# Kernel optimization log

Measured on AMD Instinct MI355X. Metric: run time of the kernel, lower is better.

The kernel has to match this reference:

```python
import jax, jax.numpy as jnp
import numpy as np

B, P, C, H, W = 256, 512, 512, 7, 8
T = H * W  # 56
EPS = 1e-8


def setup_inputs() -> dict:
    key = jax.random.key(0)
    k1, k2, k3 = jax.random.split(key, 3)
    inp = jax.random.normal(k1, (B, C, H, W), dtype=jnp.float32)
    # xavier-uniform-like init for prototype (fan over last two dims as torch does)
    bound_p = float(np.sqrt(6.0 / (P + C * T)))
    prototype = jax.random.uniform(k2, (P, C, T), dtype=jnp.float32, minval=-bound_p, maxval=bound_p)
    bound_w = float(np.sqrt(6.0 / (C + 1)))
    fc_w = jax.random.uniform(k3, (1, C), dtype=jnp.float32, minval=-bound_w, maxval=bound_w)
    fc_b = jnp.zeros((1,), dtype=jnp.float32)
    return {"input": inp, "prototype": prototype, "fc_w": fc_w, "fc_b": fc_b}


def reference(input, prototype, fc_w, fc_b):
    # flatten spatial dims: (B, C, T)
    x = input.reshape(input.shape[0], input.shape[1], -1)
    # per-position cosine similarity over channel dim
    dots = jnp.einsum('bct,pct->bpt', x, prototype)          # (B, P, T)
    xn = jnp.linalg.norm(x, axis=1)                           # (B, T)
    pn = jnp.linalg.norm(prototype, axis=1)                   # (P, T)
    sim = dots / jnp.maximum(xn[:, None, :] * pn[None, :, :], EPS)
    att = jax.nn.softmax(sim, axis=-1)                        # (B, P, T)
    # attention-pooled elementwise product: (B, P, C)
    feat = jnp.einsum('bpt,bct,pct->bpc', att, x, prototype)
    # fc: Linear(C, 1) then relu, view to (B, P)
    out = jax.nn.relu(jnp.einsum('bpc,oc->bpo', feat, fc_w) + fc_b)
    return out.reshape(out.shape[0], out.shape[1])
```

## Files before the change

### kernel.cpp

```cpp
#include <hip/hip_runtime.h>
#include <hip/hip_bf16.h>
#include <math.h>

constexpr int kB = 256, kC = 512, kT = 56, kP = 512;
constexpr int kCT = kC * kT;

typedef short v4s __attribute__((ext_vector_type(4)));
typedef short v8s __attribute__((ext_vector_type(8)));
typedef float v4f __attribute__((ext_vector_type(4)));

__device__ __forceinline__ unsigned pack_bf16(float a, float b) {
  __hip_bfloat16 ha = __float2bfloat16(a);
  __hip_bfloat16 hb = __float2bfloat16(b);
  unsigned short ua, ub;
  __builtin_memcpy(&ua, &ha, 2);
  __builtin_memcpy(&ub, &hb, 2);
  return (unsigned)ua | ((unsigned)ub << 16);
}

__device__ __forceinline__ v4s frag2(unsigned w0, unsigned w1) {
  unsigned u[2] = {w0, w1};
  v4s s;
  __builtin_memcpy(&s, u, 8);
  return s;
}

__device__ __forceinline__ v8s frag8(uint4 u) {
  v8s s;
  __builtin_memcpy(&s, &u, 16);
  return s;
}

__global__ __launch_bounds__(512) void prep_kernel(
    const float* __restrict__ x, const float* __restrict__ proto,
    const float* __restrict__ fcw,
    unsigned* __restrict__ xt, unsigned* __restrict__ xwt,
    unsigned* __restrict__ pt,
    float* __restrict__ xn, float* __restrict__ pn) {
  __shared__ float tile[512 * 57];
  __shared__ float fws[512];
  __shared__ float part[8][64];

  const int tid = threadIdx.x;
  const int n = blockIdx.x;
  const bool isx = (n < kB);
  const int row = isx ? n : (n - kB);
  const float* src = (isx ? x + (size_t)row * kCT : proto + (size_t)row * kCT);

  fws[tid] = fcw[tid & 511];

#pragma unroll 1
  for (int it = 0; it < 14; ++it) {
    const int f0 = it * 2048 + tid * 4;
    float4 v = *(const float4*)(src + f0);
#pragma unroll
    for (int j = 0; j < 4; ++j) {
      int f = f0 + j;
      int c = (int)(((unsigned)f * 74899u) >> 22);
      int t = f - c * 56;
      tile[c * 57 + t] = ((const float*)&v)[j];
    }
  }
  __syncthreads();

  {
    const int g = tid >> 6, tt = tid & 63;
    float a = 0.f;
    if (tt < 56) {
      for (int c = g * 64; c < g * 64 + 64; ++c) {
        float u = tile[c * 57 + tt];
        a = fmaf(u, u, a);
      }
    }
    part[g][tt] = a;
  }
  __syncthreads();
  if (tid < 56) {
    float s = 0.f;
#pragma unroll
    for (int g = 0; g < 8; ++g) s += part[g][tid];
    float r = sqrtf(s);
    if (isx) xn[row * 56 + tid] = r; else pn[row * 56 + tid] = r;
  }

#pragma unroll 1
  for (int it = 0; it < 28; ++it) {
    const int id = it * 512 + tid;
    const int t = id >> 8;
    const int cw = id & 255;
    float g0 = tile[(2 * cw) * 57 + t];
    float g1 = tile[(2 * cw + 1) * 57 + t];
    unsigned wd = pack_bf16(g0, g1);
    if (isx) {
      size_t o = ((size_t)(t * kB + row)) * 256 + cw;
      xt[o] = wd;
      xwt[o] = pack_bf16(g0 * fws[2 * cw], g1 * fws[2 * cw + 1]);
    } else {
      pt[((size_t)(t * kP + row)) * 256 + cw] = wd;
    }
  }
}

constexpr int TSZ = 64 * 64;
constexpr int BUF = 3 * TSZ;

__global__ __launch_bounds__(512) void proto_gemm_kernel(
    const unsigned* __restrict__ xt, const unsigned* __restrict__ xwt,
    const unsigned* __restrict__ pt,
    const float* __restrict__ xn, const float* __restrict__ pn,
    float* __restrict__ part) {
  __shared__ __align__(16) unsigned lds[2 * BUF];

  const int tid = threadIdx.x;
  const int l = tid & 63;
  const int w = tid >> 6;
  const int wm = w & 3;
  const int wn = w >> 2;
  const int b0 = blockIdx.x * 64;
  const int p0 = blockIdx.y * 64;
  const int tg = blockIdx.z;

  const int sr0 = tid >> 4;
  const int sr1 = sr0 + 32;
  const int sc = (tid & 15) * 4;
  const int lw0 = sr0 * 64 + (sc ^ ((sr0 & 7) * 4));
  const int lw1 = sr1 * 64 + (sc ^ ((sr1 & 7) * 4));

  const int fr = l & 15;
  const int q = l >> 4;
  const int sw = (fr & 7) * 4;
  const int axr = (wm * 16 + fr) * 64;
  const int ap0r = (wn * 32 + fr) * 64;
  const int ap1r = ap0r + 16 * 64;

  v4f aD0, aD1, aW0, aW1;
  aD0 = aD1 = aW0 = aW1 = v4f{0.f, 0.f, 0.f, 0.f};
  v4f m0v, m1v, s0v, s1v, n0v, n1v;
  m0v = m1v = v4f{-3.0e38f, -3.0e38f, -3.0e38f, -3.0e38f};
  s0v = s1v = n0v = n1v = v4f{0.f, 0.f, 0.f, 0.f};

  uint4 Ax0, Ax1, Aw0, Aw1, Ap0, Ap1;
  uint4 Bx0, Bx1, Bw0, Bw1, Bp0, Bp1;
  float xnv[4] = {0.f, 0.f, 0.f, 0.f};
  float pnv0 = 0.f, pnv1 = 0.f;

#define LOAD_REGS(S, CC) do { \
    const int t_ = tg * 7 + ((CC) >> 2); \
    const int w0_ = ((CC) & 3) * 64; \
    const unsigned* gx_ = xt + ((size_t)(t_ * kB + b0)) * 256 + w0_ + sc; \
    const unsigned* gw_ = xwt + ((size_t)(t_ * kB + b0)) * 256 + w0_ + sc; \
    const unsigned* gp_ = pt + ((size_t)(t_ * kP + p0)) * 256 + w0_ + sc; \
    S##x0 = *(const uint4*)(gx_ + (size_t)sr0 * 256); \
    S##x1 = *(const uint4*)(gx_ + (size_t)sr1 * 256); \
    S##w0 = *(const uint4*)(gw_ + (size_t)sr0 * 256); \
    S##w1 = *(const uint4*)(gw_ + (size_t)sr1 * 256); \
    S##p0 = *(const uint4*)(gp_ + (size_t)sr0 * 256); \
    S##p1 = *(const uint4*)(gp_ + (size_t)sr1 * 256); \
  } while (0)

#define STORE_LDS(S, CC) do { \
    unsigned* b_ = lds + ((CC) & 1) * BUF; \
    *(uint4*)(b_ + lw0) = S##x0; \
    *(uint4*)(b_ + lw1) = S##x1; \
    *(uint4*)(b_ + TSZ + lw0) = S##w0; \
    *(uint4*)(b_ + TSZ + lw1) = S##w1; \
    *(uint4*)(b_ + 2 * TSZ + lw0) = S##p0; \
    *(uint4*)(b_ + 2 * TSZ + lw1) = S##p1; \
  } while (0)

  auto compute = [&](int cc) {
    if ((cc & 3) == 0) {
      const int t = tg * 7 + (cc >> 2);
      const int brow = b0 + wm * 16 + q * 4;
#pragma unroll
      for (int i = 0; i < 4; ++i) xnv[i] = xn[(brow + i) * 56 + t];
      pnv0 = pn[(p0 + wn * 32 + fr) * 56 + t];
      pnv1 = pn[(p0 + wn * 32 + 16 + fr) * 56 + t];
    }
    const unsigned* bx = lds + (cc & 1) * BUF;
    const unsigned* bw = bx + TSZ;
    const unsigned* bp = bx + 2 * TSZ;
#pragma unroll
    for (int ks = 0; ks < 4; ++ks) {
      const int col = (ks * 16 + q * 4) ^ sw;
      uint4 xr = *(const uint4*)(bx + axr + col);
      uint4 wr = *(const uint4*)(bw + axr + col);
      uint4 p0r = *(const uint4*)(bp + ap0r + col);
      uint4 p1r = *(const uint4*)(bp + ap1r + col);
      v8s xf = frag8(xr), wf = frag8(wr), pf0 = frag8(p0r), pf1 = frag8(p1r);
      aD0 = __builtin_amdgcn_mfma_f32_16x16x32_bf16(xf, pf0, aD0, 0, 0, 0);
      aD1 = __builtin_amdgcn_mfma_f32_16x16x32_bf16(xf, pf1, aD1, 0, 0, 0);
      aW0 = __builtin_amdgcn_mfma_f32_16x16x32_bf16(wf, pf0, aW0, 0, 0, 0);
      aW1 = __builtin_amdgcn_mfma_f32_16x16x32_bf16(wf, pf1, aW1, 0, 0, 0);
    }
    if ((cc & 3) == 3) {
#pragma unroll
      for (int i = 0; i < 4; ++i) {
        {
          float den = fmaxf(xnv[i] * pnv0, 1e-8f);
          float sim = aD0[i] * __builtin_amdgcn_rcpf(den);
          float mo = m0v[i];
          float mn = fmaxf(mo, sim);
          float cs = __expf(mo - mn);
          float e = __expf(sim - mn);
          s0v[i] = s0v[i] * cs + e;
          n0v[i] = fmaf(e, aW0[i], n0v[i] * cs);
          m0v[i] = mn;
        }
        {
          float den = fmaxf(xnv[i] * pnv1, 1e-8f);
          float sim = aD1[i] * __builtin_amdgcn_rcpf(den);
          float mo = m1v[i];
          float mn = fmaxf(mo, sim);
          float cs = __expf(mo - mn);
          float e = __expf(sim - mn);
          s1v[i] = s1v[i] * cs + e;
          n1v[i] = fmaf(e, aW1[i], n1v[i] * cs);
          m1v[i] = mn;
        }
      }
      aD0 = aD1 = aW0 = aW1 = v4f{0.f, 0.f, 0.f, 0.f};
    }
  };

  LOAD_REGS(A, 0);
  STORE_LDS(A, 0);
  LOAD_REGS(B, 1);
  __syncthreads();

#pragma unroll 1
  for (int cc = 0; cc < 28; cc += 2) {
    if (cc + 1 < 28) STORE_LDS(B, cc + 1);
    if (cc + 2 < 28) LOAD_REGS(A, cc + 2);
    compute(cc);
    __syncthreads();
    if (cc + 2 < 28) STORE_LDS(A, cc + 2);
    if (cc + 3 < 28) LOAD_REGS(B, cc + 3);
    compute(cc + 1);
    __syncthreads();
  }

#undef LOAD_REGS
#undef STORE_LDS

  float* pm = part + ((size_t)tg * 3 + 0) * 131072;
  float* ps = part + ((size_t)tg * 3 + 1) * 131072;
  float* pu = part + ((size_t)tg * 3 + 2) * 131072;
#pragma unroll
  for (int i = 0; i < 4; ++i) {
    const int bg = b0 + wm * 16 + q * 4 + i;
    {
      const size_t o = (size_t)bg * 512 + p0 + wn * 32 + fr;
      pm[o] = m0v[i]; ps[o] = s0v[i]; pu[o] = n0v[i];
    }
    {
      const size_t o = (size_t)bg * 512 + p0 + wn * 32 + 16 + fr;
      pm[o] = m1v[i]; ps[o] = s1v[i]; pu[o] = n1v[i];
    }
  }
}

__global__ __launch_bounds__(256) void merge_kernel(
    const float* __restrict__ part, const float* __restrict__ fcb,
    float* __restrict__ out) {
  const int pair = blockIdx.x * 256 + threadIdx.x;
  float M = -3.0e38f;
#pragma unroll
  for (int k = 0; k < 8; ++k) M = fmaxf(M, part[((size_t)k * 3) * 131072 + pair]);
  float S = 0.f, N = 0.f;
#pragma unroll
  for (int k = 0; k < 8; ++k) {
    float mk = part[((size_t)k * 3) * 131072 + pair];
    float sc = __expf(mk - M);
    S = fmaf(part[((size_t)k * 3 + 1) * 131072 + pair], sc, S);
    N = fmaf(part[((size_t)k * 3 + 2) * 131072 + pair], sc, N);
  }
  float o = N * __builtin_amdgcn_rcpf(S) + fcb[0];
  out[pair] = fmaxf(o, 0.f);
}

__global__ __launch_bounds__(1024) void proto_mfma_kernel(
    const float* __restrict__ x, const float* __restrict__ proto,
    const float* __restrict__ fcw, const float* __restrict__ fcb,
    float* __restrict__ out) {
  __shared__ unsigned xs[56 * 289];
  __shared__ unsigned ps[56 * 145];
  __shared__ unsigned pws[56 * 145];

  const int tid = threadIdx.x;
  const int l = tid & 63;
  const int w = tid >> 6;
  const int bq = w & 1;
  const int tq = w >> 1;
  const int t0 = tq * 7;

  const int n = blockIdx.y * 32 + blockIdx.x;
  const int p0 = (n >> 3) * 16;
  const int b0 = (n & 7) * 32;

  const bool act = (l < 56);
  const int lt = l;

  const int xbase0 = ((b0 + 2 * w + 0) * kC) * kT + lt;
  const int xbase1 = ((b0 + 2 * w + 1) * kC) * kT + lt;
  const int pbase = ((p0 + w) * kC) * kT + lt;

  const int arow = l & 15;
  const int q2 = (l >> 4) << 1;
  const int xoff = (bq * 16 + arow) * 9 + q2;
  const int poff = arow * 9 + q2;

  v4f acc[7][2];
#pragma unroll
  for (int ti = 0; ti < 7; ++ti) {
    acc[ti][0] = v4f{0.f, 0.f, 0.f, 0.f};
    acc[ti][1] = v4f{0.f, 0.f, 0.f, 0.f};
  }
  float xn2a = 0.f, xn2b = 0.f, pn2 = 0.f;

#pragma unroll 1
  for (int st = 0; st < 32; ++st) {
    const int k0 = st * 16;
    if (act) {
#pragma unroll
      for (int r = 0; r < 16; ++r) {
        const int cw = r & 7;
        const int c = k0 + 2 * cw;
        const int ga = ((r >> 3) ? xbase1 : xbase0) + c * kT;
        float g0 = x[ga], g1 = x[ga + kT];
        if (r >> 3) xn2b = fmaf(g0, g0, fmaf(g1, g1, xn2b));
        else xn2a = fmaf(g0, g0, fmaf(g1, g1, xn2a));
        xs[lt * 289 + (2 * w + (r >> 3)) * 9 + cw] = pack_bf16(g0, g1);
      }
#pragma unroll
      for (int cw = 0; cw < 8; ++cw) {
        const int c = k0 + 2 * cw;
        const int ga = pbase + c * kT;
        float g0 = proto[ga], g1 = proto[ga + kT];
        pn2 = fmaf(g0, g0, fmaf(g1, g1, pn2));
        ps[lt * 145 + w * 9 + cw] = pack_bf16(g0, g1);
        float f0 = fcw[c], f1 = fcw[c + 1];
        pws[lt * 145 + w * 9 + cw] = pack_bf16(g0 * f0, g1 * f1);
      }
    }
    __syncthreads();
#pragma unroll
    for (int ti = 0; ti < 7; ++ti) {
      const int t = t0 + ti;
      unsigned xw0 = xs[t * 289 + xoff];
      unsigned xw1 = xs[t * 289 + xoff + 1];
      unsigned pw0 = ps[t * 145 + poff];
      unsigned pw1 = ps[t * 145 + poff + 1];
      unsigned ww0 = pws[t * 145 + poff];
      unsigned ww1 = pws[t * 145 + poff + 1];
      v4s af = frag2(xw0, xw1);
      v4s bf = frag2(pw0, pw1);
      v4s wf = frag2(ww0, ww1);
      acc[ti][0] = __builtin_amdgcn_mfma_f32_16x16x16bf16_1k(af, bf, acc[ti][0], 0, 0, 0);
      acc[ti][1] = __builtin_amdgcn_mfma_f32_16x16x16bf16_1k(af, wf, acc[ti][1], 0, 0, 0);
    }
    __syncthreads();
  }

  float* xnorm = (float*)ps;
  float* pnorm = xnorm + 32 * 56;
  if (act) {
    xnorm[(2 * w + 0) * 56 + lt] = xn2a;
    xnorm[(2 * w + 1) * 56 + lt] = xn2b;
    pnorm[w * 56 + lt] = pn2;
  }
  __syncthreads();

  float* fm = (float*)xs;
  float* fsum = fm + 4096;
  float* fnum = fsum + 4096;
  const int pc = arow;
  const int qq = l >> 4;
#pragma unroll
  for (int i = 0; i < 4; ++i) {
    const int bl = bq * 16 + 4 * qq + i;
    float m = -3.0e38f;
    float sims[7];
#pragma unroll
    for (int ti = 0; ti < 7; ++ti) {
      const int t = t0 + ti;
      float den = fmaxf(sqrtf(xnorm[bl * 56 + t]) * sqrtf(pnorm[pc * 56 + t]), 1e-8f);
      float s = acc[ti][0][i] / den;
      sims[ti] = s;
      m = fmaxf(m, s);
    }
    float se = 0.f, nu = 0.f;
#pragma unroll
    for (int ti = 0; ti < 7; ++ti) {
      float e = __expf(sims[ti] - m);
      se += e;
      nu = fmaf(e, acc[ti][1][i], nu);
    }
    const int pair = bl * 16 + pc;
    fm[tq * 512 + pair] = m;
    fsum[tq * 512 + pair] = se;
    fnum[tq * 512 + pair] = nu;
  }
  __syncthreads();

  if (tid < 512) {
    float M = -3.0e38f;
#pragma unroll
    for (int k = 0; k < 8; ++k) M = fmaxf(M, fm[k * 512 + tid]);
    float S = 0.f, N = 0.f;
#pragma unroll
    for (int k = 0; k < 8; ++k) {
      float sc = __expf(fm[k * 512 + tid] - M);
      S = fmaf(fsum[k * 512 + tid], sc, S);
      N = fmaf(fnum[k * 512 + tid], sc, N);
    }
    float o = N / S + fcb[0];
    out[(b0 + (tid >> 4)) * kP + p0 + (tid & 15)] = fmaxf(o, 0.f);
  }
}

extern "C" void kernel_launch(void* const* d_in, const int* in_sizes, int n_in,
                              void* d_out, int out_size, void* d_ws, size_t ws_size,
                              hipStream_t stream) {
  const float* x = (const float*)d_in[0];
  const float* proto = (const float*)d_in[1];
  const float* fcw = (const float*)d_in[2];
  const float* fcb = (const float*)d_in[3];
  float* out = (float*)d_out;

  const size_t need = 71475200;
  if (ws_size >= need) {
    unsigned* xt = (unsigned*)d_ws;
    unsigned* xwt = xt + 3670016;
    unsigned* ptb = xt + 7340032;
    float* partb = (float*)(xt + 14680064);
    float* xnb = (float*)(xt + 17825792);
    float* pnb = (float*)(xt + 17840128);

    hipLaunchKernelGGL(prep_kernel, dim3(kB + kP), dim3(512), 0, stream,
                       x, proto, fcw, xt, xwt, ptb, xnb, pnb);
    hipLaunchKernelGGL(proto_gemm_kernel, dim3(4, 8, 8), dim3(512), 0, stream,
                       xt, xwt, ptb, xnb, pnb, partb);
    hipLaunchKernelGGL(merge_kernel, dim3(512), dim3(256), 0, stream,
                       partb, fcb, out);
  } else {
    hipLaunchKernelGGL(proto_mfma_kernel, dim3(32, 8), dim3(1024), 0, stream,
                       x, proto, fcw, fcb, out);
  }
}
```

Before: 73.54 us.

## Process prep transpose in 128-channel chunks to shrink LDS footprint

The prep kernel now stages one 128-channel slice of each row at a time instead of the whole 512x56 tile. This cuts shared memory from about 114KB to about 29KB so several blocks can be resident per CU. The norm accumulation and the bf16 transpose writes are done per chunk. In exchange it adds extra barriers per chunk, and the loads are unrolled with the four float4 components computed from a single channel/time index.

```diff
diff --git a/kernel.cpp b/kernel.cpp
--- a/kernel.cpp
+++ b/kernel.cpp
@@ -37,7 +37,7 @@
     unsigned* __restrict__ xt, unsigned* __restrict__ xwt,
     unsigned* __restrict__ pt,
     float* __restrict__ xn, float* __restrict__ pn) {
-  __shared__ float tile[512 * 57];
+  __shared__ float tile[128 * 57];
   __shared__ float fws[512];
   __shared__ float part[8][64];
 
@@ -45,59 +45,66 @@
   const int n = blockIdx.x;
   const bool isx = (n < kB);
   const int row = isx ? n : (n - kB);
-  const float* src = (isx ? x + (size_t)row * kCT : proto + (size_t)row * kCT);
+  const float* src = (isx ? x : proto) + (size_t)row * kCT;
 
   fws[tid] = fcw[tid & 511];
 
+  const int g = tid >> 6, tt = tid & 63;
+  float nacc = 0.f;
+
 #pragma unroll 1
-  for (int it = 0; it < 14; ++it) {
-    const int f0 = it * 2048 + tid * 4;
-    float4 v = *(const float4*)(src + f0);
-#pragma unroll
-    for (int j = 0; j < 4; ++j) {
-      int f = f0 + j;
-      int c = (int)(((unsigned)f * 74899u) >> 22);
-      int t = f - c * 56;
-      tile[c * 57 + t] = ((const float*)&v)[j];
-    }
-  }
-  __syncthreads();
-
-  {
-    const int g = tid >> 6, tt = tid & 63;
-    float a = 0.f;
+  for (int ch = 0; ch < 4; ++ch) {
+    const float* csrc = src + ch * (128 * 56);
+#pragma unroll
+    for (int it = 0; it < 4; ++it) {
+      const int idx = it * 512 + tid;
+      if (idx < 1792) {
+        const int f0 = idx * 4;
+        float4 v = *(const float4*)(csrc + f0);
+        int c = (int)(((unsigned)f0 * 74899u) >> 22);
+        int t = f0 - c * 56;
+        tile[c * 57 + t] = v.x;
+        tile[c * 57 + t + 1] = v.y;
+        tile[c * 57 + t + 2] = v.z;
+        tile[c * 57 + t + 3] = v.w;
+      }
+    }
+    __syncthreads();
     if (tt < 56) {
-      for (int c = g * 64; c < g * 64 + 64; ++c) {
-        float u = tile[c * 57 + tt];
-        a = fmaf(u, u, a);
-      }
-    }
-    part[g][tt] = a;
-  }
+#pragma unroll
+      for (int cc2 = 0; cc2 < 16; ++cc2) {
+        float u = tile[(g * 16 + cc2) * 57 + tt];
+        nacc = fmaf(u, u, nacc);
+      }
+    }
+#pragma unroll
+    for (int it = 0; it < 7; ++it) {
+      const int id = it * 512 + tid;
+      const int t = id >> 6;
+      const int cw = id & 63;
+      float g0 = tile[(2 * cw) * 57 + t];
+      float g1 = tile[(2 * cw + 1) * 57 + t];
+      unsigned wd = pack_bf16(g0, g1);
+      if (isx) {
+        size_t o = ((size_t)(t * kB + row)) * 256 + ch * 64 + cw;
+        xt[o] = wd;
+        const int c = ch * 128 + 2 * cw;
+        xwt[o] = pack_bf16(g0 * fws[c], g1 * fws[c + 1]);
+      } else {
+        pt[((size_t)(t * kP + row)) * 256 + ch * 64 + cw] = wd;
+      }
+    }
+    __syncthreads();
+  }
+
+  part[g][tt] = nacc;
   __syncthreads();
   if (tid < 56) {
     float s = 0.f;
 #pragma unroll
-    for (int g = 0; g < 8; ++g) s += part[g][tid];
+    for (int gg = 0; gg < 8; ++gg) s += part[gg][tid];
     float r = sqrtf(s);
     if (isx) xn[row * 56 + tid] = r; else pn[row * 56 + tid] = r;
-  }
-
-#pragma unroll 1
-  for (int it = 0; it < 28; ++it) {
-    const int id = it * 512 + tid;
-    const int t = id >> 8;
-    const int cw = id & 255;
-    float g0 = tile[(2 * cw) * 57 + t];
-    float g1 = tile[(2 * cw + 1) * 57 + t];
-    unsigned wd = pack_bf16(g0, g1);
-    if (isx) {
-      size_t o = ((size_t)(t * kB + row)) * 256 + cw;
-      xt[o] = wd;
-      xwt[o] = pack_bf16(g0 * fws[2 * cw], g1 * fws[2 * cw + 1]);
-    } else {
-      pt[((size_t)(t * kP + row)) * 256 + cw] = wd;
-    }
   }
 }
 
```

After: 65.27 us. 11.2% less time.
